# Kernel optimization log

Measured on AMD Instinct MI355X. Metric: run time of the kernel, lower is better.

## Reference

```python
import jax, jax.numpy as jnp
import numpy as np
from jax import lax

DN = ('NDHWC', 'DHWIO', 'NDHWC')
SHAPE = (33, 33, 33)
B = 2
N = 40000
C = 64


def setup_inputs() -> dict:
    key = jax.random.key(0)
    ks = jax.random.split(key, 24)
    D, H, W = SHAPE
    # unique active voxel coords (batch, z, y, x)
    rng = np.random.default_rng(0)
    idx = rng.choice(B * D * H * W, size=N, replace=False)
    b = idx // (D * H * W)
    r = idx % (D * H * W)
    coors = np.stack([b, r // (H * W), (r // W) % H, r % W], axis=1).astype(np.int32)

    def w(k, shape, scale=0.1):
        return jax.random.normal(k, shape, jnp.float32) * scale

    inp = {
        'features': jax.random.normal(ks[0], (N, 3), jnp.float32),
        'coors': jnp.asarray(coors),
        'batch_size': B,
        'w1': w(ks[1], (3, 3, 3, 3, C), 0.2), 'b1': w(ks[2], (C,), 0.05),
        'w2': w(ks[3], (3, 3, 3, C, C), 0.05), 'b2': w(ks[4], (C,), 0.05),
        'w3': w(ks[5], (3, 3, 3, C, C), 0.05), 'b3': w(ks[6], (C,), 0.05),
        'wt': w(ks[7], (3, 3, 3, C, C), 0.05), 'bt': w(ks[8], (C,), 0.05),
        'w5': w(ks[9], (3, 3, 3, C, C), 0.05), 'b5': w(ks[10], (C,), 0.05),
    }
    # folded eval-mode BatchNorm: y = x*s + h  (s = gamma/sqrt(var+eps), h = beta - mean*s)
    for i, (sk, hk) in enumerate(zip(ks[11:16], ks[16:21]), start=1):
        inp[f's{i}'] = 1.0 + 0.1 * jax.random.normal(sk, (C,), jnp.float32)
        inp[f'h{i}'] = 0.05 * jax.random.normal(hk, (C,), jnp.float32)
    return inp


def _forward(features, coors, batch_size,
             w1, b1, w2, b2, w3, b3, wt, bt, w5, b5,
             s1, h1, s2, h2, s3, h3, s4, h4, s5, h5):
    D, H, W = SHAPE
    bi, zi, yi, xi = coors[:, 0], coors[:, 1], coors[:, 2], coors[:, 3]
    # densify SparseConvTensor (zeros at inactive sites) + active mask
    x = jnp.zeros((batch_size, D, H, W, features.shape[-1]), features.dtype)
    x = x.at[bi, zi, yi, xi].set(features)
    m = jnp.zeros((batch_size, D, H, W, 1), jnp.float32).at[bi, zi, yi, xi].set(1.0)
    ones3 = jnp.ones((3, 3, 3, 1, 1), jnp.float32)

    conv = lambda a, k, pad: lax.conv_general_dilated(a, k, (1, 1, 1), pad, dimension_numbers=DN)
    # masked BN(eval) + ReLU: applied only on active sites, background stays exactly 0
    act = lambda y, mm, s, h: jnp.where(mm, jax.nn.relu(y * s + h), 0.0)

    # SparseConv3d(3,64,3): valid conv; output actives = 1-dilation of input actives
    x = conv(x, w1, 'VALID')
    m1 = conv(m, ones3, 'VALID') > 0  # [B,31,31,31,1]
    x = act(x + b1, m1, s1, h1)

    # two SubMConv3d(64,64,3) sharing indice_key: same active set, SAME padding
    x = act(conv(x, w2, 'SAME') + b2, m1, s2, h2)
    x = act(conv(x, w3, 'SAME') + b3, m1, s3, h3)

    # SparseConvTranspose3d(64,64,3,2): out = (D-1)*2+3; actives = transposed dilation
    x = lax.conv_transpose(x, wt, (2, 2, 2), 'VALID', dimension_numbers=DN)
    mT = lax.conv_transpose(m1.astype(jnp.float32), ones3, (2, 2, 2), 'VALID', dimension_numbers=DN) > 0
    x = act(x + bt, mT, s4, h4)

    # ToDense -> dense Conv3d(64,64,3) -> BN -> ReLU (dense: applied everywhere)
    x = conv(x, w5, 'VALID') + b5
    x = jax.nn.relu(x * s5 + h5)
    return jnp.transpose(x, (0, 4, 1, 2, 3))  # NCDHW like spconv ToDense output


def reference(features, coors, batch_size,
              w1, b1, w2, b2, w3, b3, wt, bt, w5, b5,
              s1, h1, s2, h2, s3, h3, s4, h4, s5, h5):
    return _forward(features, coors, batch_size,
                    w1, b1, w2, b2, w3, b3, wt, bt, w5, b5,
                    s1, h1, s2, h2, s3, h3, s4, h4, s5, h5)
```

## Files before the change

kernel.cpp:

```cpp
#include <hip/hip_runtime.h>
#include <cstdint>

constexpr int BB = 2, C = 64;
constexpr int D1 = 31;
constexpr int DP = 33;
constexpr int D4 = 63;
constexpr int D5 = 61;
constexpr int D5CUBE = D5*D5*D5;

constexpr int NV1 = BB*D1*D1*D1;
constexpr int NVP = BB*DP*DP*DP;
constexpr int NV4 = BB*D4*D4*D4;
constexpr int NV5 = BB*D5*D5*D5;

constexpr size_t alup(size_t x) { return (x + 255) & ~(size_t)255; }
constexpr size_t OB_X0  = 0;
constexpr size_t OB_M0  = alup(OB_X0  + (size_t)NVP*3*4);
constexpr size_t OB_M1P = alup(OB_M0  + (size_t)NVP*4);
constexpr size_t OB_X1  = alup(OB_M1P + (size_t)NVP*4);
constexpr size_t OB_X2  = alup(OB_X1  + (size_t)NVP*64*2);
constexpr size_t OB_X3  = alup(OB_X2  + (size_t)NVP*64*2);
constexpr size_t OB_MT  = alup(OB_X3  + (size_t)NVP*64*2);
constexpr size_t OB_X4  = alup(OB_MT  + (size_t)NV4*4);
constexpr size_t OB_WB2 = alup(OB_X4  + (size_t)NV4*64*2);
constexpr size_t OB_WB3 = alup(OB_WB2 + (size_t)27*64*64*2);
constexpr size_t OB_WBT = alup(OB_WB3 + (size_t)27*64*64*2);
constexpr size_t OB_WB5 = alup(OB_WBT + (size_t)27*64*64*2);

typedef __attribute__((ext_vector_type(8))) short short8;
typedef __attribute__((ext_vector_type(4))) float f32x4;

__device__ inline unsigned short f2bf(float f) {
  unsigned int u = __float_as_uint(f);
  u = (u + 0x7FFFu + ((u >> 16) & 1u)) >> 16;
  return (unsigned short)u;
}

template<int DD>
__device__ inline void decodev(int vox, int& b, int& z, int& y, int& x) {
  x = vox % DD; int r = vox / DD;
  y = r % DD;   r /= DD;
  z = r % DD;   b = r / DD;
}

__device__ inline int xcd_swz(int bid, int nb) {
  int q = nb >> 3, r = nb & 7;
  int xcd = bid & 7, idx = bid >> 3;
  return (xcd < r ? xcd*(q+1) : r*(q+1) + (xcd - r)*q) + idx;
}

__global__ void __launch_bounds__(256)
k_zero(float* __restrict__ x0, float* __restrict__ m0, float* __restrict__ m1p,
       unsigned short* __restrict__ x1, unsigned short* __restrict__ x2,
       unsigned short* __restrict__ x3) {
  int v = blockIdx.x*256 + threadIdx.x;
  if (v >= NVP) return;
  m0[v] = 0.f; m1p[v] = 0.f;
  x0[3*v+0] = 0.f; x0[3*v+1] = 0.f; x0[3*v+2] = 0.f;
  int x = v % DP, r = v / DP;
  int y = r % DP; r /= DP;
  int z = r % DP;
  if (x==0 || x==DP-1 || y==0 || y==DP-1 || z==0 || z==DP-1) {
    ulonglong2 zz = {0ull, 0ull};
    ulonglong2* p1 = (ulonglong2*)(x1 + (size_t)v*64);
    ulonglong2* p2 = (ulonglong2*)(x2 + (size_t)v*64);
    ulonglong2* p3 = (ulonglong2*)(x3 + (size_t)v*64);
    #pragma unroll
    for (int i = 0; i < 8; i++) { p1[i] = zz; p2[i] = zz; p3[i] = zz; }
  }
}

__global__ void k_scatter(const float* __restrict__ feat, const int* __restrict__ coors,
                          int n, float* __restrict__ x0, float* __restrict__ m0) {
  int i = blockIdx.x*blockDim.x + threadIdx.x;
  if (i >= n) return;
  int b = coors[4*i+0], z = coors[4*i+1], y = coors[4*i+2], x = coors[4*i+3];
  int v = ((b*DP + z)*DP + y)*DP + x;
  x0[v*3+0] = feat[3*i+0];
  x0[v*3+1] = feat[3*i+1];
  x0[v*3+2] = feat[3*i+2];
  m0[v] = 1.0f;
}

__global__ void __launch_bounds__(256)
k_conv1(const float* __restrict__ x0, const float* __restrict__ m0,
        unsigned short* __restrict__ x1, float* __restrict__ m1p,
        const float* __restrict__ w1, const float* __restrict__ b1,
        const float* __restrict__ s1, const float* __restrict__ h1) {
  long long t = (long long)blockIdx.x*blockDim.x + threadIdx.x;
  if (t >= (long long)NV1*C) return;
  int co  = (int)(t & 63);
  int vox = (int)(t >> 6);
  int b, z, y, x; decodev<D1>(vox, b, z, y, x);
  float sum = 0.f, mm = 0.f;
  #pragma unroll
  for (int kz=0; kz<3; kz++)
  #pragma unroll
  for (int ky=0; ky<3; ky++)
  #pragma unroll
  for (int kx=0; kx<3; kx++) {
    int iv = ((b*DP + z+kz)*DP + y+ky)*DP + (x+kx);
    mm += m0[iv];
    const float* px = x0 + iv*3;
    const float* pw = w1 + ((kz*3+ky)*3+kx)*3*64 + co;
    sum += px[0]*pw[0] + px[1]*pw[64] + px[2]*pw[128];
  }
  bool m = mm > 0.f;
  float o = m ? fmaxf((sum + b1[co])*s1[co] + h1[co], 0.f) : 0.f;
  size_t pOff = (size_t)(((b*DP + z+1)*DP + y+1)*DP + (x+1));
  x1[pOff*C + co] = f2bf(o);
  if (co == 0) m1p[pOff] = m ? 1.f : 0.f;
}

__global__ void k_repack4(const float* __restrict__ wa, const float* __restrict__ wb,
                          const float* __restrict__ wc, const float* __restrict__ wd,
                          unsigned short* __restrict__ da, unsigned short* __restrict__ db,
                          unsigned short* __restrict__ dc, unsigned short* __restrict__ dd) {
  int which = blockIdx.x / 432;
  int i = (blockIdx.x - which*432)*256 + threadIdx.x;
  const float* w = which == 0 ? wa : which == 1 ? wb : which == 2 ? wc : wd;
  unsigned short* dst = which == 0 ? da : which == 1 ? db : which == 2 ? dc : dd;
  int co = i & 63, k = (i >> 6) & 63, t = i >> 12;
  int kk = k >> 5, q = (k >> 3) & 3, j = k & 7, cb = co >> 4, l = q*16 + (co & 15);
  dst[(size_t)((t*2+kk)*4+cb)*512 + l*8 + j] = f2bf(w[i]);
}

template<int NA, int DOUT, int DIN>
__global__ void __launch_bounds__(256)
k_conv_mfma(const unsigned short* __restrict__ inBF, const unsigned short* __restrict__ wB,
            unsigned short* __restrict__ outPtr, const float* __restrict__ m1p,
            const float* __restrict__ bias, const float* __restrict__ s,
            const float* __restrict__ h) {
  constexpr int NVOX = BB*DOUT*DOUT*DOUT;
  const int lane = threadIdx.x & 63;
  const int wid  = threadIdx.x >> 6;
  const int wave = xcd_swz(blockIdx.x, gridDim.x)*4 + wid;
  const int vb   = wave * (NA*16);

  int rowb[NA];
  #pragma unroll
  for (int a = 0; a < NA; a++) {
    int vox = vb + a*16 + (lane & 15);
    vox = vox < NVOX ? vox : NVOX-1;
    int b, z, y, x; decodev<DOUT>(vox, b, z, y, x);
    rowb[a] = (((b*DIN + z)*DIN + y)*DIN + x)*64;
  }
  const int koff = (lane >> 4) * 8;

  f32x4 acc[NA][4];
  #pragma unroll
  for (int a = 0; a < NA; a++)
    #pragma unroll
    for (int cb = 0; cb < 4; cb++)
      acc[a][cb] = f32x4{0.f, 0.f, 0.f, 0.f};

  #pragma unroll 1
  for (int t = 0; t < 27; ++t) {
    int kz = t / 9, rr = t - kz*9;
    int ky = rr / 3, kx = rr - ky*3;
    const int toff = ((kz*DIN + ky)*DIN + kx)*64;
    #pragma unroll
    for (int kk = 0; kk < 2; ++kk) {
      short8 A[NA];
      #pragma unroll
      for (int a = 0; a < NA; a++)
        A[a] = *reinterpret_cast<const short8*>(inBF + rowb[a] + toff + kk*32 + koff);
      short8 Bv[4];
      const unsigned short* wp = wB + (size_t)(t*2+kk)*2048 + lane*8;
      #pragma unroll
      for (int cb = 0; cb < 4; cb++)
        Bv[cb] = *reinterpret_cast<const short8*>(wp + cb*512);
      #pragma unroll
      for (int a = 0; a < NA; a++)
        #pragma unroll
        for (int cb = 0; cb < 4; cb++)
          acc[a][cb] = __builtin_amdgcn_mfma_f32_16x16x32_bf16(A[a], Bv[cb], acc[a][cb], 0, 0, 0);
    }
  }

  float bv[4], sv[4], hv[4];
  #pragma unroll
  for (int cb = 0; cb < 4; cb++) {
    int c = cb*16 + (lane & 15);
    bv[cb] = bias[c]; sv[cb] = s[c]; hv[cb] = h[c];
  }

  #pragma unroll
  for (int a = 0; a < NA; a++)
    #pragma unroll
    for (int r = 0; r < 4; r++) {
      int vox = vb + a*16 + (lane >> 4)*4 + r;
      if (vox >= NVOX) continue;
      int b, z, y, x; decodev<DOUT>(vox, b, z, y, x);
      size_t pOff = (size_t)(((b*DP + z+1)*DP + y+1)*DP + (x+1));
      bool m = m1p[pOff] > 0.f;
      #pragma unroll
      for (int cb = 0; cb < 4; cb++) {
        float o = m ? fmaxf((acc[a][cb][r] + bv[cb])*sv[cb] + hv[cb], 0.f) : 0.f;
        outPtr[pOff*64 + cb*16 + (lane & 15)] = f2bf(o);
      }
    }
}

__global__ void __launch_bounds__(256)
k_maskT(const float* __restrict__ m1p, float* __restrict__ mt) {
  int vox = blockIdx.x*256 + threadIdx.x;
  if (vox >= NV4) return;
  int b, zo, yo, xo; decodev<D4>(vox, b, zo, yo, xo);
  float mm = 0.f;
  for (int kz = 0; kz < 3; kz++) {
    if ((zo + kz) & 1) continue;
    int izp = ((zo + kz - 2) >> 1) + 1;
    for (int ky = 0; ky < 3; ky++) {
      if ((yo + ky) & 1) continue;
      int iyp = ((yo + ky - 2) >> 1) + 1;
      for (int kx = 0; kx < 3; kx++) {
        if ((xo + kx) & 1) continue;
        int ixp = ((xo + kx - 2) >> 1) + 1;
        mm += m1p[((b*DP + izp)*DP + iyp)*DP + ixp];
      }
    }
  }
  mt[vox] = mm;
}

__global__ void __launch_bounds__(256)
k_convT_mfma(const unsigned short* __restrict__ x3, const unsigned short* __restrict__ wB,
             unsigned short* __restrict__ x4, const float* __restrict__ mt,
             const float* __restrict__ bias, const float* __restrict__ s,
             const float* __restrict__ h) {
  const int lane = threadIdx.x & 63;
  const int wid  = threadIdx.x >> 6;
  const int w    = xcd_swz(blockIdx.x, gridDim.x)*4 + wid;
  if (w >= BB*D4*D4) return;
  const int b  = w / (D4*D4);
  const int rm = w % (D4*D4);
  const int zo = rm / D4;
  const int yo = rm % D4;
  const int ii = lane & 15;
  const int koff = (lane >> 4) * 8;

  f32x4 acc[4][4];
  #pragma unroll
  for (int a = 0; a < 4; a++)
    #pragma unroll
    for (int cb = 0; cb < 4; cb++)
      acc[a][cb] = f32x4{0.f, 0.f, 0.f, 0.f};

  #pragma unroll 1
  for (int kz = 0; kz < 3; kz++) {
    if ((zo + kz) & 1) continue;
    const int izp = ((zo + kz - 2) >> 1) + 1;
    #pragma unroll 1
    for (int ky = 0; ky < 3; ky++) {
      if ((yo + ky) & 1) continue;
      const int iyp = ((yo + ky - 2) >> 1) + 1;
      const size_t planeBase = ((size_t)((b*DP + izp)*DP + iyp))*DP*64;
      #pragma unroll
      for (int kx = 0; kx < 3; kx++) {
        const int apar  = kx & 1;
        const int xoffE = ((kx + apar - 2) >> 1) + 1;
        const int t = (kz*3 + ky)*3 + kx;
        #pragma unroll
        for (int kk = 0; kk < 2; ++kk) {
          short8 Bv[4];
          const unsigned short* wpk = wB + (size_t)(t*2+kk)*2048 + lane*8;
          #pragma unroll
          for (int cb = 0; cb < 4; cb++)
            Bv[cb] = *reinterpret_cast<const short8*>(wpk + cb*512);
          #pragma unroll
          for (int ablk = 0; ablk < 2; ablk++) {
            const int ixp = ablk*16 + ii + xoffE;
            short8 A = *reinterpret_cast<const short8*>(x3 + planeBase + (size_t)ixp*64 + kk*32 + koff);
            const int afr = apar*2 + ablk;
            #pragma unroll
            for (int cb = 0; cb < 4; cb++)
              acc[afr][cb] = __builtin_amdgcn_mfma_f32_16x16x32_bf16(A, Bv[cb], acc[afr][cb], 0, 0, 0);
          }
        }
      }
    }
  }

  float bv[4], sv[4], hv[4];
  #pragma unroll
  for (int cb = 0; cb < 4; cb++) {
    int c = cb*16 + (lane & 15);
    bv[cb] = bias[c]; sv[cb] = s[c]; hv[cb] = h[c];
  }
  const int rowBase = ((b*D4 + zo)*D4 + yo)*D4;
  #pragma unroll
  for (int a = 0; a < 4; a++) {
    const int ablk = a & 1, apar = a >> 1;
    #pragma unroll
    for (int r = 0; r < 4; r++) {
      const int row = (lane >> 4)*4 + r;
      const int xo  = 2*(ablk*16 + row) + apar;
      if (xo >= D4) continue;
      const int vox = rowBase + xo;
      const bool m = mt[vox] > 0.f;
      #pragma unroll
      for (int cb = 0; cb < 4; cb++) {
        float o = m ? fmaxf((acc[a][cb][r] + bv[cb])*sv[cb] + hv[cb], 0.f) : 0.f;
        x4[(size_t)vox*64 + cb*16 + (lane & 15)] = f2bf(o);
      }
    }
  }
}

__device__ __forceinline__ void c5_step(const short8 (&A)[4], const short8 (&W)[4],
                                        f32x4 (&acc)[4][4]) {
  #pragma unroll
  for (int a = 0; a < 4; a++)
    #pragma unroll
    for (int cb = 0; cb < 4; cb++)
      acc[a][cb] = __builtin_amdgcn_mfma_f32_16x16x32_bf16(W[cb], A[a], acc[a][cb], 0, 0, 0);
}

__global__ void __launch_bounds__(256, 2)
k_conv5_mfma(const unsigned short* __restrict__ x4, const unsigned short* __restrict__ wB,
             float* __restrict__ out, const float* __restrict__ bias,
             const float* __restrict__ s, const float* __restrict__ h) {
  __shared__ short8 sA[2][2048];
  const int tid  = threadIdx.x;
  const int lane = tid & 63;
  const int wid  = tid >> 6;
  const int ll   = lane & 15;
  const int l16  = lane >> 4;

  const int blk   = xcd_swz(blockIdx.x, gridDim.x);
  const int ytile = blk & 15;
  const int rzb   = blk >> 4;
  const int z     = rzb % D5;
  const int b     = rzb / D5;
  const int y0    = ytile * 4;

  int st_r[8], st_base[8];
  #pragma unroll
  for (int it = 0; it < 8; ++it) {
    int g = it*256 + tid; g = g > 2015 ? 2015 : g;
    int r = g / 504, rem = g - r*504;
    int v = rem >> 3, c16p = rem & 7;
    int c16l = c16p ^ (v & 7);
    st_r[it] = r;
    st_base[it] = (v << 7) + (c16l << 4);
  }

  const char* x4b = (const char*)x4;

  f32x4 acc[4][4];
  #pragma unroll
  for (int a = 0; a < 4; a++)
    #pragma unroll
    for (int cb = 0; cb < 4; cb++)
      acc[a][cb] = f32x4{0.f, 0.f, 0.f, 0.f};

  auto STAGE_A = [&](int kzn, int kyn, int hn) {
    size_t pb = (size_t)(b*D4 + z + kzn) * (D4*D4*128);
    char* dst = (char*)&sA[hn][0];
    #pragma unroll
    for (int it = 0; it < 8; ++it) {
      int yin = y0 + st_r[it] + kyn; yin = yin > 62 ? 62 : yin;
      __builtin_amdgcn_global_load_lds(
        (const __attribute__((address_space(1))) void*)(x4b + pb + (size_t)yin*8064 + st_base[it]),
        (__attribute__((address_space(3))) void*)(dst + it*4096 + wid*1024),
        16, 0, 0);
    }
  };
  auto LDA = [&](int hh, int kx, int kk, short8 (&A)[4]) {
    #pragma unroll
    for (int a = 0; a < 4; a++) {
      int v  = a*16 + ll + kx;
      int ch = wid*504 + v*8 + ((kk*4 + l16) ^ (v & 7));
      A[a] = sA[hh][ch];
    }
  };

  short8 A0[4], A1[4];

  STAGE_A(0, 0, 0);
  __syncthreads();

  int kzn = 0, kyn = 1;
  #pragma unroll 1
  for (int p = 0; p < 9; ++p) {
    const int hh = p & 1;

    short8 W[6][4];
    {
      const unsigned short* wp = wB + (size_t)p*12288 + lane*8;
      #pragma unroll
      for (int st = 0; st < 6; ++st)
        #pragma unroll
        for (int cb = 0; cb < 4; cb++)
          W[st][cb] = *reinterpret_cast<const short8*>(wp + st*2048 + cb*512);
    }
    __builtin_amdgcn_sched_barrier(0);

    if (p < 8) {
      STAGE_A(kzn, kyn, hh ^ 1);
      kyn++; if (kyn == 3) { kyn = 0; kzn++; }
    }
    __builtin_amdgcn_sched_barrier(0);

    LDA(hh, 0, 0, A0);
    #pragma unroll
    for (int st = 0; st < 6; ++st) {
      const int kxn = (st+1) >> 1, kkn = (st+1) & 1;
      if (st < 5) {
        if (st & 1) LDA(hh, kxn, kkn, A0); else LDA(hh, kxn, kkn, A1);
      }
      if (st & 1) c5_step(A1, W[st], acc); else c5_step(A0, W[st], acc);
    }
    __syncthreads();
  }

  const int yout = y0 + wid;
  if (yout < D5) {
    #pragma unroll
    for (int a = 0; a < 4; a++) {
      int x = a*16 + ll;
      if (x >= D5) continue;
      size_t sp = (size_t)(z*D5 + yout)*D5 + x;
      #pragma unroll
      for (int cb = 0; cb < 4; cb++)
        #pragma unroll
        for (int r = 0; r < 4; r++) {
          int co = cb*16 + l16*4 + r;
          float o = fmaxf((acc[a][cb][r] + bias[co])*s[co] + h[co], 0.f);
          out[(size_t)(b*64 + co)*D5CUBE + sp] = o;
        }
    }
  }
}

extern "C" void kernel_launch(void* const* d_in, const int* in_sizes, int n_in,
                              void* d_out, int out_size, void* d_ws, size_t ws_size,
                              hipStream_t stream) {
  const float* feat  = (const float*)d_in[0];
  const int*   coors = (const int*)d_in[1];
  const float* w1 = (const float*)d_in[3];
  const float* b1 = (const float*)d_in[4];
  const float* w2 = (const float*)d_in[5];
  const float* b2 = (const float*)d_in[6];
  const float* w3 = (const float*)d_in[7];
  const float* b3 = (const float*)d_in[8];
  const float* wt = (const float*)d_in[9];
  const float* bt = (const float*)d_in[10];
  const float* w5 = (const float*)d_in[11];
  const float* b5 = (const float*)d_in[12];
  const float* s1 = (const float*)d_in[13];
  const float* h1 = (const float*)d_in[14];
  const float* s2 = (const float*)d_in[15];
  const float* h2 = (const float*)d_in[16];
  const float* s3 = (const float*)d_in[17];
  const float* h3 = (const float*)d_in[18];
  const float* s4 = (const float*)d_in[19];
  const float* h4 = (const float*)d_in[20];
  const float* s5 = (const float*)d_in[21];
  const float* h5 = (const float*)d_in[22];
  int n = in_sizes[0] / 3;

  char* wsb = (char*)d_ws;
  float*          X0  = (float*)(wsb + OB_X0);
  float*          M0  = (float*)(wsb + OB_M0);
  float*          M1P = (float*)(wsb + OB_M1P);
  unsigned short* X1  = (unsigned short*)(wsb + OB_X1);
  unsigned short* X2  = (unsigned short*)(wsb + OB_X2);
  unsigned short* X3  = (unsigned short*)(wsb + OB_X3);
  float*          MT  = (float*)(wsb + OB_MT);
  unsigned short* X4  = (unsigned short*)(wsb + OB_X4);
  unsigned short* WB2 = (unsigned short*)(wsb + OB_WB2);
  unsigned short* WB3 = (unsigned short*)(wsb + OB_WB3);
  unsigned short* WBT = (unsigned short*)(wsb + OB_WBT);
  unsigned short* WB5 = (unsigned short*)(wsb + OB_WB5);

  k_zero<<<(NVP + 255)/256, 256, 0, stream>>>(X0, M0, M1P, X1, X2, X3);

  k_repack4<<<1728, 256, 0, stream>>>(w2, w3, wt, w5, WB2, WB3, WBT, WB5);

  k_scatter<<<(n+255)/256, 256, 0, stream>>>(feat, coors, n, X0, M0);

  {
    long long threads = (long long)NV1*C;
    k_conv1<<<(int)((threads+255)/256), 256, 0, stream>>>(X0, M0, X1, M1P, w1, b1, s1, h1);
  }

  constexpr int WAVES23 = (NV1 + 31) / 32;
  constexpr int BLK23   = (WAVES23 + 3) / 4;
  k_conv_mfma<2, D1, DP><<<BLK23, 256, 0, stream>>>(X1, WB2, X2, M1P, b2, s2, h2);
  k_conv_mfma<2, D1, DP><<<BLK23, 256, 0, stream>>>(X2, WB3, X3, M1P, b3, s3, h3);

  k_maskT<<<(NV4 + 255)/256, 256, 0, stream>>>(M1P, MT);

  constexpr int ROWS_T = BB*D4*D4;
  k_convT_mfma<<<(ROWS_T + 3)/4, 256, 0, stream>>>(X3, WBT, X4, MT, bt, s4, h4);

  constexpr int BLK5 = BB * D5 * 16;
  k_conv5_mfma<<<BLK5, 256, 0, stream>>>(X4, WB5, (float*)d_out, b5, s5, h5);
}
```

Measured before the change: 362.5 us.

## Split conv5 tiles along x to halve accumulators and raise occupancy

The final dense conv kernel now splits each output row into two 32-wide x tiles, which doubles the grid. Each wave keeps 2x4 accumulator tiles instead of 4x4, and stages only its own input row into a smaller LDS buffer. Launch bounds go from 2 to 4 blocks per CU. Weights are loaded in two halves of three steps each instead of all six up front, and s_setprio is placed around the MFMA bursts. The aim is to cut register and LDS pressure so more waves can hide memory latency, at the cost of reading every weight twice as often per output and staging overlapping input halos.

```diff
diff --git a/kernel.cpp b/kernel.cpp
--- a/kernel.cpp
+++ b/kernel.cpp
@@ -308,77 +308,85 @@
   }
 }
 
-__device__ __forceinline__ void c5_step(const short8 (&A)[4], const short8 (&W)[4],
-                                        f32x4 (&acc)[4][4]) {
-  #pragma unroll
-  for (int a = 0; a < 4; a++)
+__device__ __forceinline__ void c5_step2(const short8 (&A)[2], const short8 (&W)[4],
+                                         f32x4 (&acc)[2][4]) {
+  #pragma unroll
+  for (int a = 0; a < 2; a++)
     #pragma unroll
     for (int cb = 0; cb < 4; cb++)
       acc[a][cb] = __builtin_amdgcn_mfma_f32_16x16x32_bf16(W[cb], A[a], acc[a][cb], 0, 0, 0);
 }
 
-__global__ void __launch_bounds__(256, 2)
+__global__ void __launch_bounds__(256, 4)
 k_conv5_mfma(const unsigned short* __restrict__ x4, const unsigned short* __restrict__ wB,
              float* __restrict__ out, const float* __restrict__ bias,
              const float* __restrict__ s, const float* __restrict__ h) {
-  __shared__ short8 sA[2][2048];
+  __shared__ short8 sA[2][1280];
   const int tid  = threadIdx.x;
   const int lane = tid & 63;
   const int wid  = tid >> 6;
   const int ll   = lane & 15;
   const int l16  = lane >> 4;
 
-  const int blk   = xcd_swz(blockIdx.x, gridDim.x);
-  const int ytile = blk & 15;
-  const int rzb   = blk >> 4;
-  const int z     = rzb % D5;
-  const int b     = rzb / D5;
-  const int y0    = ytile * 4;
-
-  int st_r[8], st_base[8];
-  #pragma unroll
-  for (int it = 0; it < 8; ++it) {
-    int g = it*256 + tid; g = g > 2015 ? 2015 : g;
-    int r = g / 504, rem = g - r*504;
-    int v = rem >> 3, c16p = rem & 7;
+  const int blk = xcd_swz(blockIdx.x, gridDim.x);
+  const int xt  = blk & 1;
+  const int yt  = (blk >> 1) & 15;
+  const int rzb = blk >> 5;
+  const int z   = rzb % D5;
+  const int b   = rzb / D5;
+  const int y0  = yt * 4;
+  const int xbase = xt * 32;
+
+  int st_off[5];
+  #pragma unroll
+  for (int it = 0; it < 5; ++it) {
+    int g = it*64 + lane;
+    int v = g >> 3, c16p = g & 7;
     int c16l = c16p ^ (v & 7);
-    st_r[it] = r;
-    st_base[it] = (v << 7) + (c16l << 4);
+    st_off[it] = xt*4096 + (v << 7) + (c16l << 4);
   }
 
   const char* x4b = (const char*)x4;
 
-  f32x4 acc[4][4];
-  #pragma unroll
-  for (int a = 0; a < 4; a++)
+  f32x4 acc[2][4];
+  #pragma unroll
+  for (int a = 0; a < 2; a++)
     #pragma unroll
     for (int cb = 0; cb < 4; cb++)
       acc[a][cb] = f32x4{0.f, 0.f, 0.f, 0.f};
 
-  auto STAGE_A = [&](int kzn, int kyn, int hn) {
-    size_t pb = (size_t)(b*D4 + z + kzn) * (D4*D4*128);
-    char* dst = (char*)&sA[hn][0];
-    #pragma unroll
-    for (int it = 0; it < 8; ++it) {
-      int yin = y0 + st_r[it] + kyn; yin = yin > 62 ? 62 : yin;
+  auto STAGE = [&](int kzn, int kyn, int hn) {
+    int yin = y0 + kyn + wid; yin = yin > 62 ? 62 : yin;
+    size_t rb = ((size_t)((b*D4 + z + kzn)*D4 + yin)) * 8064;
+    char* dst = (char*)&sA[hn][0] + wid*5120;
+    #pragma unroll
+    for (int it = 0; it < 5; ++it) {
       __builtin_amdgcn_global_load_lds(
-        (const __attribute__((address_space(1))) void*)(x4b + pb + (size_t)yin*8064 + st_base[it]),
-        (__attribute__((address_space(3))) void*)(dst + it*4096 + wid*1024),
+        (const __attribute__((address_space(1))) void*)(x4b + rb + st_off[it]),
+        (__attribute__((address_space(3))) void*)(dst + it*1024),
         16, 0, 0);
     }
   };
-  auto LDA = [&](int hh, int kx, int kk, short8 (&A)[4]) {
-    #pragma unroll
-    for (int a = 0; a < 4; a++) {
-      int v  = a*16 + ll + kx;
-      int ch = wid*504 + v*8 + ((kk*4 + l16) ^ (v & 7));
-      A[a] = sA[hh][ch];
+  auto LDA = [&](int hh, int kx, int kk, short8 (&A)[2]) {
+    #pragma unroll
+    for (int a = 0; a < 2; a++) {
+      int v = a*16 + ll + kx;
+      int ch = hh*1280 + wid*320 + v*8 + ((kk*4 + l16) ^ (v & 7));
+      A[a] = sA[0][ch];
     }
   };
-
-  short8 A0[4], A1[4];
-
-  STAGE_A(0, 0, 0);
+  auto LDW3 = [&](int slot0, short8 (&W)[3][4]) {
+    const unsigned short* wp = wB + (size_t)slot0*2048 + lane*8;
+    #pragma unroll
+    for (int st = 0; st < 3; ++st)
+      #pragma unroll
+      for (int cb = 0; cb < 4; cb++)
+        W[st][cb] = *reinterpret_cast<const short8*>(wp + st*2048 + cb*512);
+  };
+
+  short8 A0[2], A1[2];
+
+  STAGE(0, 0, 0);
   __syncthreads();
 
   int kzn = 0, kyn = 1;
@@ -386,40 +394,45 @@
   for (int p = 0; p < 9; ++p) {
     const int hh = p & 1;
 
-    short8 W[6][4];
-    {
-      const unsigned short* wp = wB + (size_t)p*12288 + lane*8;
-      #pragma unroll
-      for (int st = 0; st < 6; ++st)
-        #pragma unroll
-        for (int cb = 0; cb < 4; cb++)
-          W[st][cb] = *reinterpret_cast<const short8*>(wp + st*2048 + cb*512);
-    }
+    short8 Wa[3][4];
+    LDW3(p*6 + 0, Wa);
     __builtin_amdgcn_sched_barrier(0);
-
     if (p < 8) {
-      STAGE_A(kzn, kyn, hh ^ 1);
+      STAGE(kzn, kyn, hh ^ 1);
       kyn++; if (kyn == 3) { kyn = 0; kzn++; }
     }
     __builtin_amdgcn_sched_barrier(0);
 
     LDA(hh, 0, 0, A0);
-    #pragma unroll
-    for (int st = 0; st < 6; ++st) {
-      const int kxn = (st+1) >> 1, kkn = (st+1) & 1;
-      if (st < 5) {
-        if (st & 1) LDA(hh, kxn, kkn, A0); else LDA(hh, kxn, kkn, A1);
-      }
-      if (st & 1) c5_step(A1, W[st], acc); else c5_step(A0, W[st], acc);
-    }
+    __builtin_amdgcn_s_setprio(1);
+    LDA(hh, 0, 1, A1);
+    c5_step2(A0, Wa[0], acc);
+    LDA(hh, 1, 0, A0);
+    c5_step2(A1, Wa[1], acc);
+    LDA(hh, 1, 1, A1);
+    c5_step2(A0, Wa[2], acc);
+    __builtin_amdgcn_s_setprio(0);
+
+    short8 Wb[3][4];
+    LDW3(p*6 + 3, Wb);
+    __builtin_amdgcn_sched_barrier(0);
+
+    LDA(hh, 2, 0, A0);
+    __builtin_amdgcn_s_setprio(1);
+    c5_step2(A1, Wb[0], acc);
+    LDA(hh, 2, 1, A1);
+    c5_step2(A0, Wb[1], acc);
+    c5_step2(A1, Wb[2], acc);
+    __builtin_amdgcn_s_setprio(0);
+
     __syncthreads();
   }
 
   const int yout = y0 + wid;
   if (yout < D5) {
     #pragma unroll
-    for (int a = 0; a < 4; a++) {
-      int x = a*16 + ll;
+    for (int a = 0; a < 2; a++) {
+      int x = xbase + a*16 + ll;
       if (x >= D5) continue;
       size_t sp = (size_t)(z*D5 + yout)*D5 + x;
       #pragma unroll
@@ -496,6 +509,6 @@
   constexpr int ROWS_T = BB*D4*D4;
   k_convT_mfma<<<(ROWS_T + 3)/4, 256, 0, stream>>>(X3, WBT, X4, MT, bt, s4, h4);
 
-  constexpr int BLK5 = BB * D5 * 16;
+  constexpr int BLK5 = BB * D5 * 16 * 2;
   k_conv5_mfma<<<BLK5, 256, 0, stream>>>(X4, WB5, (float*)d_out, b5, s5, h5);
 }
```

Result: slower. 395.2 us (+9.0%).
